# Optimization experiments

Measured on AMD Instinct MI355X. Metric: run time of the kernel, lower is better.

Reference implementation:

```python
import jax, jax.numpy as jnp
import numpy as np

B, N, L = 32, 50, 16384  # batch, n_templates, segment length
KT = 4096                # template kernel length


def conv1d(x, w, pad, groups=1):
    # x: [B, Cin, L], w: [Cout, Cin/groups, K] (torch layout)
    return jax.lax.conv_general_dilated(
        x, w, window_strides=(1,), padding=[(pad, pad)],
        dimension_numbers=('NCH', 'OIH', 'NCH'), feature_group_count=groups)


def maxpool3(x):
    # MaxPool1d(kernel=3, stride=3), floor mode (VALID)
    return jax.lax.reduce_window(x, -jnp.inf, jax.lax.max,
                                 (1, 1, 3), (1, 1, 3), 'VALID')


def pad_to(x, m):
    p = (-x.shape[-1]) % m
    pads = ((0, 0),) * (x.ndim - 1) + ((0, p),)
    return jnp.pad(x, pads)


def setup_inputs() -> dict:
    key = jax.random.key(0)
    ks = jax.random.split(key, 12)
    return dict(
        xi=jax.random.normal(ks[0], (B, 2, L), jnp.float32),
        S_t_m12=jax.random.normal(ks[1], (2, 1, L), jnp.float32) * 0.01,
        template=jax.random.normal(ks[2], (N, 2, KT), jnp.float32) * 0.01,
        hh_sqrt=jax.random.uniform(ks[3], (N, 2), jnp.float32) + 0.5,
        W1=jax.random.normal(ks[4], (16, 2, 3), jnp.float32) * 0.1,
        b1=jnp.zeros((16,), jnp.float32),
        W2=jax.random.normal(ks[5], (32, 16, 3), jnp.float32) * 0.1,
        b2=jnp.zeros((32,), jnp.float32),
        W3=jax.random.normal(ks[6], (32, 128), jnp.float32) * 0.1,
        b3=jnp.zeros((32,), jnp.float32),
        W4=jax.random.normal(ks[7], (2, 32), jnp.float32) * 0.1,
        b4=jnp.zeros((2,), jnp.float32),
    )


def reference(xi, S_t_m12, template, hh_sqrt, W1, b1, W2, b2, W3, b3, W4, b4):
    # Whitening matched filter: grouped conv with kernel length L
    y = conv1d(xi, S_t_m12, L - 1, groups=2)          # [B, 2, 2L-1]
    y = pad_to(y, L)                                   # [B, 2, 2L]
    # wrap-fold each channel: reshape(B,2,L).sum over the fold axis
    d_SA = y[:, 0].reshape(-1, 2, L).sum(1)[:, None, :]  # [B,1,L]
    d_SE = y[:, 1].reshape(-1, 2, L).sum(1)[:, None, :]
    h_SA = template[:, 0, :].reshape(-1, 1, KT)          # [N,1,KT]
    h_SE = template[:, 1, :].reshape(-1, 1, KT)
    dh_A = pad_to(conv1d(d_SA, h_SA, KT - 1), L).reshape(-1, N, 2, L).sum(2)  # [B,N,L]
    dh_E = pad_to(conv1d(d_SE, h_SE, KT - 1), L).reshape(-1, N, 2, L).sum(2)
    z = jnp.stack((dh_A, dh_E), -1).transpose(0, 2, 1, 3)  # [B,L,N,2]
    z = z / hh_sqrt                                         # broadcast [N,2]
    z = z.max(axis=1).transpose(0, 2, 1)                    # [B,2,N]
    # small CNN + MLP head
    h = maxpool3(jax.nn.sigmoid(conv1d(z, W1, 0) + b1[None, :, None]))  # [B,16,16]
    h = maxpool3(jax.nn.sigmoid(conv1d(h, W2, 0) + b2[None, :, None]))  # [B,32,4]
    h = h.reshape(h.shape[0], -1)                                        # [B,128]
    h = jax.nn.relu(h @ W3.T + b3)
    return h @ W4.T + b4                                                 # [B,2]
```

## Files before the change

### kernel.cpp

```cpp
#include <hip/hip_runtime.h>
#include <math.h>

#define L_LEN 16384
#define M_LEN 8192
#define KT_LEN 4096
#define BB 32
#define NTPL 50
#define SPEC_STRIDE 8224
#define NSIG 166
#define NT 512
#define PI_F 3.14159265358979323846f
#define C16 0.98078528040323044f
#define S16 0.19509032201612827f

typedef float cf2 __attribute__((ext_vector_type(2)));

__device__ __forceinline__ cf2 cmul(cf2 a, cf2 b) {
    cf2 byx = __builtin_shufflevector(b, b, 1, 0);
    return (cf2){a.x, a.x} * b + (cf2){-a.y, a.y} * byx;
}
__device__ __forceinline__ cf2 cmulc(cf2 a, cf2 b) {
    return a * (cf2){b.x, b.x} + (cf2){a.y, -a.x} * (cf2){b.y, b.y};
}
template<int SIGN>
__device__ __forceinline__ cf2 rot90(cf2 z) {
    return (SIGN < 0) ? (cf2){z.y, -z.x} : (cf2){-z.y, z.x};
}
template<int SIGN>
__device__ __forceinline__ cf2 ldT(const cf2* __restrict__ T, int idx) {
    cf2 t = T[idx];
    if (SIGN > 0) t.y = -t.y;
    return t;
}

__device__ __forceinline__ int swz(int i) { return i ^ (((i >> 5) & 15) << 1); }

__device__ __forceinline__ int pos(int f) {
    return ((f & 15) << 9) | (((f >> 4) & 15) << 5) |
           (((f >> 8) & 15) << 1) | ((f >> 12) & 1);
}

template<int SIGN>
__device__ __forceinline__ void dft16(cf2 x[16]) {
    const float S = (SIGN < 0) ? -1.f : 1.f;
    const cf2 w1 = {0.9238795325112867f, S * 0.3826834323650898f};
    const cf2 w2 = {0.7071067811865476f, S * 0.7071067811865476f};
    const cf2 w3 = {0.3826834323650898f, S * 0.9238795325112867f};
    cf2 v[16];
    #pragma unroll
    for (int n1 = 0; n1 < 4; ++n1) {
        cf2 a0 = x[n1], a1 = x[n1+4], a2 = x[n1+8], a3 = x[n1+12];
        cf2 t0 = a0 + a2, t2 = a0 - a2;
        cf2 t1 = a1 + a3, t3 = rot90<SIGN>(a1 - a3);
        cf2 u0 = t0 + t1, u1 = t2 + t3;
        cf2 u2 = t0 - t1, u3 = t2 - t3;
        if (n1 == 1) { u1 = cmul(u1, w1); u2 = cmul(u2, w2); u3 = cmul(u3, w3); }
        else if (n1 == 2) { u1 = cmul(u1, w2); u2 = rot90<SIGN>(u2);
                            u3 = rot90<SIGN>(cmul(u3, w2)); }
        else if (n1 == 3) { u1 = cmul(u1, w3); u2 = rot90<SIGN>(cmul(u2, w2));
                            u3 = -cmul(u3, w1); }
        v[0*4+n1] = u0; v[1*4+n1] = u1; v[2*4+n1] = u2; v[3*4+n1] = u3;
    }
    #pragma unroll
    for (int r = 0; r < 4; ++r) {
        cf2 a0 = v[r*4+0], a1 = v[r*4+1], a2 = v[r*4+2], a3 = v[r*4+3];
        cf2 t0 = a0 + a2, t2 = a0 - a2;
        cf2 t1 = a1 + a3, t3 = rot90<SIGN>(a1 - a3);
        x[r]    = t0 + t1; x[r+4]  = t2 + t3;
        x[r+8]  = t0 - t1; x[r+12] = t2 - t3;
    }
}

template<int SIGN>
__device__ __forceinline__ void butterfly16(cf2* A, const int idx[16], cf2 w1) {
    cf2 x[16];
    #pragma unroll
    for (int n = 0; n < 16; ++n) x[n] = A[idx[n]];
    dft16<SIGN>(x);
    A[idx[0]] = x[0];
    A[idx[1]] = cmul(x[1], w1);
    const cf2 w2 = cmul(w1, w1);
    A[idx[2]] = cmul(x[2], w2);
    const cf2 w3 = cmul(w1, w2);
    A[idx[3]] = cmul(x[3], w3);
    const cf2 w4 = cmul(w2, w2);
    A[idx[4]] = cmul(x[4], w4);
    A[idx[5]] = cmul(x[5], cmul(w1, w4));
    A[idx[6]] = cmul(x[6], cmul(w2, w4));
    A[idx[7]] = cmul(x[7], cmul(w3, w4));
    const cf2 w8 = cmul(w4, w4);
    A[idx[8]]  = cmul(x[8],  w8);
    A[idx[9]]  = cmul(x[9],  cmul(w1, w8));
    A[idx[10]] = cmul(x[10], cmul(w2, w8));
    A[idx[11]] = cmul(x[11], cmul(w3, w8));
    const cf2 w12 = cmul(w4, w8);
    A[idx[12]] = cmul(x[12], w12);
    A[idx[13]] = cmul(x[13], cmul(w1, w12));
    A[idx[14]] = cmul(x[14], cmul(w2, w12));
    A[idx[15]] = cmul(x[15], cmul(w3, w12));
}


__global__ __launch_bounds__(NT, 4)
void fwd_fft_kernel(const float* __restrict__ xi, const float* __restrict__ w,
                    const float* __restrict__ tmpl, cf2* __restrict__ Tw,
                    cf2* __restrict__ spec) {
    __shared__ __attribute__((aligned(16))) cf2 A[M_LEN];
    const int sig = blockIdx.x;
    const int tid = threadIdx.x;

    if (sig >= NSIG) {
        const int k = (sig - NSIG) * NT + tid;
        const double a = -M_PI * (double)k / 8192.0;
        Tw[k] = (cf2){(float)cos(a), (float)sin(a)};
        return;
    }

    const float* src;
    int nre;
    if (sig < 64)      { src = xi   + sig * L_LEN;         nre = L_LEN; }
    else if (sig < 66) { src = w    + (sig - 64) * L_LEN;  nre = L_LEN; }
    else               { src = tmpl + (sig - 66) * KT_LEN; nre = KT_LEN; }
    const int nc = nre >> 1;
    const float4* s4 = (const float4*)src;
    const int g0 = tid ^ ((tid >> 4) & 15);
    #pragma unroll
    for (int m = 0; m < 8; ++m) {
        const int u = 2*tid + 1024*m;
        float4 vv = (u < nc) ? s4[tid + 512*m] : make_float4(0.f, 0.f, 0.f, 0.f);
        ((float4*)A)[g0 + 512*m] = vv;
    }
    __syncthreads();

    {
        int idx[16]; const int b0 = swz(tid);
        #pragma unroll
        for (int n = 0; n < 16; ++n) idx[n] = b0 + 512*n;
        float sn, cs; __sincosf(-PI_F * (float)(2*tid) / 8192.f, &sn, &cs);
        butterfly16<-1>(A, idx, (cf2){cs, sn});
    }
    __syncthreads();
    {
        const int blk = tid >> 5, j = tid & 31, jb = blk*512;
        int idx[16];
        #pragma unroll
        for (int n = 0; n < 16; ++n) idx[n] = jb + 32*n + (j ^ (2*n));
        float sn, cs; __sincosf(-PI_F * (float)(32*j) / 8192.f, &sn, &cs);
        butterfly16<-1>(A, idx, (cf2){cs, sn});
    }
    __syncthreads();
    {
        const int blk = tid >> 1, j = tid & 1;
        const int xv = (blk & 15) << 1, b3 = blk*32 + j;
        int idx[16];
        #pragma unroll
        for (int n = 0; n < 16; ++n) idx[n] = b3 + ((2*n) ^ xv);
        cf2 w1 = j ? (cf2){C16, -S16} : (cf2){1.f, 0.f};
        butterfly16<-1>(A, idx, w1);
    }
    __syncthreads();
    #pragma unroll
    for (int m = 0; m < 8; ++m) {
        float4 pq = ((float4*)A)[g0 + 512*m];
        ((float4*)A)[g0 + 512*m] = make_float4(pq.x + pq.z, pq.y + pq.w,
                                               pq.x - pq.z, pq.y - pq.w);
    }
    __syncthreads();

    cf2* out = spec + (size_t)sig * SPEC_STRIDE;
    #pragma unroll
    for (int m = 0; m < 16; ++m) {
        const int f = tid + 512*m;
        const int fb = (M_LEN - f) & (M_LEN - 1);
        cf2 Za = A[swz(pos(f))];
        cf2 Zb = A[swz(pos(fb))];
        cf2 E = (cf2){0.5f*(Za.x + Zb.x), 0.5f*(Za.y - Zb.y)};
        cf2 D = (cf2){Za.x - Zb.x, Za.y + Zb.y};
        cf2 O = (cf2){0.5f*D.y, -0.5f*D.x};
        float sn, cs;
        __sincosf(-PI_F * (float)f / 8192.f, &sn, &cs);
        cf2 TO = (cf2){cs*O.x - sn*O.y, cs*O.y + sn*O.x};
        out[f] = E + TO;
    }
    if (tid == 0) {
        cf2 Za = A[swz(0)];
        out[M_LEN] = (cf2){Za.x - Za.y, 0.f};
    }
}

__global__ __launch_bounds__(512)
void premul_kernel(const cf2* __restrict__ T, cf2* __restrict__ spec) {
    const int bc = blockIdx.x;
    const int tid = threadIdx.x;
    const int c = bc & 1;
    cf2* Xs = spec + (size_t)bc * SPEC_STRIDE;
    const cf2* Ws = spec + (size_t)(64 + c) * SPEC_STRIDE;
    const int r = tid & 3;
    for (int f = tid; f <= M_LEN; f += 512) {
        cf2 t = cmulc(Xs[f], Ws[f]);
        cf2 p = T[(2*f) & (L_LEN - 1)];
        cf2 s = cmulc(t, p);
        cf2 o;
        if (r == 0)      o = s;
        else if (r == 1) o = (cf2){s.y, -s.x};
        else if (r == 2) o = -s;
        else             o = (cf2){-s.y, s.x};
        Xs[f] = o;
    }
}

__global__ __launch_bounds__(NT, 4)
void inv_fft_kernel(const cf2* __restrict__ spec, const cf2* __restrict__ T,
                    const float* __restrict__ hh, float* __restrict__ zarr) {
    __shared__ __attribute__((aligned(16))) cf2 A[M_LEN];
    const int idx0 = blockIdx.x;
    const int c = idx0 & 1;
    const int n = (idx0 >> 1) % NTPL;
    const int b = idx0 / (2 * NTPL);
    const int tid = threadIdx.x;

    const cf2* Ds = spec + (size_t)(b*2 + c)      * SPEC_STRIDE;
    const cf2* Hs = spec + (size_t)(66 + n*2 + c) * SPEC_STRIDE;
    const float4* D4 = (const float4*)Ds;
    const float4* H4 = (const float4*)Hs;
    const float4* T4 = (const float4*)T;
    const int g0 = tid ^ ((tid >> 4) & 15);

    #pragma unroll
    for (int m = 0; m < 4; ++m) {
        const int u = 2*tid + 1024*m;
        float4 df = D4[tid + 512*m], hf = H4[tid + 512*m];
        cf2 Sa0 = cmulc((cf2){df.x, df.y}, (cf2){hf.x, hf.y});
        cf2 Sa1 = cmulc((cf2){df.z, df.w}, (cf2){hf.z, hf.w});
        cf2 Sb0 = cmulc(Ds[M_LEN - u],     Hs[M_LEN - u]);
        cf2 Sb1 = cmulc(Ds[M_LEN - 1 - u], Hs[M_LEN - 1 - u]);
        float4 tw = T4[tid + 512*m];
        float cs0 = tw.x, sn0 = -tw.y;
        float Ex0 = 0.5f*(Sa0.x + Sb0.x), Ey0 = 0.5f*(Sa0.y - Sb0.y);
        float Dx0 = Sa0.x - Sb0.x,        Dy0 = Sa0.y + Sb0.y;
        float Ox0 = 0.5f*(cs0*Dx0 - sn0*Dy0), Oy0 = 0.5f*(cs0*Dy0 + sn0*Dx0);
        float cs1 = tw.z, sn1 = -tw.w;
        float Ex1 = 0.5f*(Sa1.x + Sb1.x), Ey1 = 0.5f*(Sa1.y - Sb1.y);
        float Dx1 = Sa1.x - Sb1.x,        Dy1 = Sa1.y + Sb1.y;
        float Ox1 = 0.5f*(cs1*Dx1 - sn1*Dy1), Oy1 = 0.5f*(cs1*Dy1 + sn1*Dx1);
        ((float4*)A)[g0 + 512*m] = make_float4(Ex0 - Oy0, Ey0 + Ox0,
                                               Ex1 - Oy1, Ey1 + Ox1);
        if (u > 0) A[swz(M_LEN - u)] = (cf2){Ex0 + Oy0, Ox0 - Ey0};
        A[swz(M_LEN - 1 - u)] = (cf2){Ex1 + Oy1, Ox1 - Ey1};
    }
    if (tid == 0) {
        cf2 S = cmulc(Ds[4096], Hs[4096]);
        A[swz(4096)] = (cf2){S.x, -S.y};
    }
    __syncthreads();

    {
        int idx[16]; const int b0 = swz(tid);
        #pragma unroll
        for (int nn = 0; nn < 16; ++nn) idx[nn] = b0 + 512*nn;
        butterfly16<+1>(A, idx, ldT<+1>(T, 2*tid));
    }
    __syncthreads();
    {
        const int blk = tid >> 5, j = tid & 31, jb = blk*512;
        int idx[16];
        #pragma unroll
        for (int nn = 0; nn < 16; ++nn) idx[nn] = jb + 32*nn + (j ^ (2*nn));
        butterfly16<+1>(A, idx, ldT<+1>(T, 32*j));
    }
    __syncthreads();

    float mx = -INFINITY;
    {
        const int blk = tid >> 1, j = tid & 1;
        const int xv = (blk & 15) << 1, b3 = blk*32 + j;
        cf2 x[16];
        #pragma unroll
        for (int nn = 0; nn < 16; ++nn) x[nn] = A[b3 + ((2*nn) ^ xv)];
        dft16<+1>(x);
        cf2 w1 = j ? (cf2){C16, S16} : (cf2){1.f, 0.f};
        auto acc = [&](cf2 z) {
            float qx = __shfl_xor(z.x, 1), qy = __shfl_xor(z.y, 1);
            float sx = z.x + qx, sy = z.y + qy;
            float dx = j ? qx - z.x : z.x - qx;
            float dy = j ? qy - z.y : z.y - qy;
            mx = fmaxf(mx, fmaxf(fmaxf(sx, sy), fmaxf(dx, dy)));
        };
        acc(x[0]);
        acc(cmul(x[1], w1));
        const cf2 w2 = cmul(w1, w1);
        acc(cmul(x[2], w2));
        const cf2 w3 = cmul(w1, w2);
        acc(cmul(x[3], w3));
        const cf2 w4 = cmul(w2, w2);
        acc(cmul(x[4], w4));
        acc(cmul(x[5], cmul(w1, w4)));
        acc(cmul(x[6], cmul(w2, w4)));
        acc(cmul(x[7], cmul(w3, w4)));
        const cf2 w8 = cmul(w4, w4);
        acc(cmul(x[8],  w8));
        acc(cmul(x[9],  cmul(w1, w8)));
        acc(cmul(x[10], cmul(w2, w8)));
        acc(cmul(x[11], cmul(w3, w8)));
        const cf2 w12 = cmul(w4, w8);
        acc(cmul(x[12], w12));
        acc(cmul(x[13], cmul(w1, w12)));
        acc(cmul(x[14], cmul(w2, w12)));
        acc(cmul(x[15], cmul(w3, w12)));
    }
    for (int off = 32; off > 0; off >>= 1)
        mx = fmaxf(mx, __shfl_xor(mx, off));
    __syncthreads();
    const int lane = tid & 63, wv = tid >> 6;
    float* redf = (float*)A;
    if (lane == 0) redf[wv] = mx;
    __syncthreads();
    if (tid == 0) {
        float mm = redf[0];
        for (int i = 1; i < NT/64; ++i) mm = fmaxf(mm, redf[i]);
        zarr[(b*2 + c)*NTPL + n] = mm / ((float)M_LEN * hh[n*2 + c]);
    }
}

__global__ __launch_bounds__(256)
void head_kernel(const float* __restrict__ zarr,
                 const float* __restrict__ W1, const float* __restrict__ b1,
                 const float* __restrict__ W2, const float* __restrict__ b2,
                 const float* __restrict__ W3, const float* __restrict__ b3,
                 const float* __restrict__ W4, const float* __restrict__ b4,
                 float* __restrict__ out) {
    __shared__ float zl[2][NTPL];
    __shared__ float s1[16][48];
    __shared__ float p1[16][16];
    __shared__ float s2[32][14];
    __shared__ float hflat[128];
    __shared__ float h1[32];
    const int b = blockIdx.x, tid = threadIdx.x;

    for (int i = tid; i < 2*NTPL; i += 256) zl[i/NTPL][i%NTPL] = zarr[b*2*NTPL + i];
    __syncthreads();
    for (int i = tid; i < 16*48; i += 256) {
        const int o = i / 48, t = i % 48;
        float acc = b1[o];
        #pragma unroll
        for (int cc = 0; cc < 2; ++cc)
            #pragma unroll
            for (int k = 0; k < 3; ++k)
                acc += zl[cc][t+k] * W1[o*6 + cc*3 + k];
        s1[o][t] = 1.f / (1.f + __expf(-acc));
    }
    __syncthreads();
    for (int i = tid; i < 16*16; i += 256) {
        const int o = i / 16, u = i % 16;
        p1[o][u] = fmaxf(fmaxf(s1[o][3*u], s1[o][3*u+1]), s1[o][3*u+2]);
    }
    __syncthreads();
    for (int i = tid; i < 32*14; i += 256) {
        const int o = i / 14, t = i % 14;
        float acc = b2[o];
        for (int cc = 0; cc < 16; ++cc)
            #pragma unroll
            for (int k = 0; k < 3; ++k)
                acc += p1[cc][t+k] * W2[o*48 + cc*3 + k];
        s2[o][t] = 1.f / (1.f + __expf(-acc));
    }
    __syncthreads();
    for (int i = tid; i < 128; i += 256) {
        const int o = i / 4, u = i % 4;
        hflat[i] = fmaxf(fmaxf(s2[o][3*u], s2[o][3*u+1]), s2[o][3*u+2]);
    }
    __syncthreads();
    if (tid < 32) {
        float acc = b3[tid];
        for (int j = 0; j < 128; ++j) acc += hflat[j] * W3[tid*128 + j];
        h1[tid] = fmaxf(acc, 0.f);
    }
    __syncthreads();
    if (tid < 2) {
        float acc = b4[tid];
        for (int j = 0; j < 32; ++j) acc += h1[j] * W4[tid*32 + j];
        out[b*2 + tid] = acc;
    }
}

extern "C" void kernel_launch(void* const* d_in, const int* in_sizes, int n_in,
                              void* d_out, int out_size, void* d_ws, size_t ws_size,
                              hipStream_t stream) {
    const float* xi   = (const float*)d_in[0];
    const float* Sw   = (const float*)d_in[1];
    const float* tmpl = (const float*)d_in[2];
    const float* hh   = (const float*)d_in[3];
    const float* W1   = (const float*)d_in[4];
    const float* b1   = (const float*)d_in[5];
    const float* W2   = (const float*)d_in[6];
    const float* b2   = (const float*)d_in[7];
    const float* W3   = (const float*)d_in[8];
    const float* b3   = (const float*)d_in[9];
    const float* W4   = (const float*)d_in[10];
    const float* b4   = (const float*)d_in[11];
    float* out = (float*)d_out;

    cf2* T16  = (cf2*)d_ws;
    cf2* spec = T16 + 16384;
    float* zarr = (float*)(spec + (size_t)NSIG * SPEC_STRIDE);

    fwd_fft_kernel<<<dim3(NSIG + 32), dim3(NT), 0, stream>>>(xi, Sw, tmpl, T16, spec);
    premul_kernel<<<dim3(64), dim3(512), 0, stream>>>(T16, spec);
    inv_fft_kernel<<<dim3(BB * NTPL * 2), dim3(NT), 0, stream>>>(spec, T16, hh, zarr);
    head_kernel<<<dim3(BB), dim3(256), 0, stream>>>(zarr, W1, b1, W2, b2, W3, b3, W4, b4, out);
}
```

Before: 165.1 us.

## Fold whitening premultiply into forward and inverse FFT kernels, drop premul launch

Removes the separate premul kernel. The phase-ramp and conjugation are folded into the whitening-filter spectrum at forward-FFT time, and the X*V product is computed on the fly inside every inverse-FFT block. The final radix stage in the inverse FFT is also swapped from a register dft16 with shuffle-based max to a shared-memory butterfly followed by a float4 scan for the max. This saves one launch and a read/write pass over the spectrum, at the cost of an extra spectrum load and complex multiply in each of the 3200 inverse blocks, plus an extra LDS round trip and barrier.

```diff
diff --git a/kernel.cpp b/kernel.cpp
--- a/kernel.cpp
+++ b/kernel.cpp
@@ -14,6 +14,7 @@
 #define S16 0.19509032201612827f
 
 typedef float cf2 __attribute__((ext_vector_type(2)));
+
 
 __device__ __forceinline__ cf2 cmul(cf2 a, cf2 b) {
     cf2 byx = __builtin_shufflevector(b, b, 1, 0);
@@ -121,6 +122,7 @@
     if (sig < 64)      { src = xi   + sig * L_LEN;         nre = L_LEN; }
     else if (sig < 66) { src = w    + (sig - 64) * L_LEN;  nre = L_LEN; }
     else               { src = tmpl + (sig - 66) * KT_LEN; nre = KT_LEN; }
+    const bool isW = (sig >= 64 && sig < 66);
     const int nc = nre >> 1;
     const float4* s4 = (const float4*)src;
     const int g0 = tid ^ ((tid >> 4) & 15);
@@ -179,33 +181,21 @@
         cf2 O = (cf2){0.5f*D.y, -0.5f*D.x};
         float sn, cs;
         __sincosf(-PI_F * (float)f / 8192.f, &sn, &cs);
-        cf2 TO = (cf2){cs*O.x - sn*O.y, cs*O.y + sn*O.x};
-        out[f] = E + TO;
+        cf2 val = E + (cf2){cs*O.x - sn*O.y, cs*O.y + sn*O.x};
+        if (isW) {
+            const int k = (4094 * f) & (L_LEN - 1);
+            float psn, pcs; __sincosf(-PI_F * (float)k / 8192.f, &psn, &pcs);
+            val = cmul((cf2){val.x, -val.y}, (cf2){pcs, psn});
+        }
+        out[f] = val;
     }
     if (tid == 0) {
         cf2 Za = A[swz(0)];
-        out[M_LEN] = (cf2){Za.x - Za.y, 0.f};
-    }
-}
-
-__global__ __launch_bounds__(512)
-void premul_kernel(const cf2* __restrict__ T, cf2* __restrict__ spec) {
-    const int bc = blockIdx.x;
-    const int tid = threadIdx.x;
-    const int c = bc & 1;
-    cf2* Xs = spec + (size_t)bc * SPEC_STRIDE;
-    const cf2* Ws = spec + (size_t)(64 + c) * SPEC_STRIDE;
-    const int r = tid & 3;
-    for (int f = tid; f <= M_LEN; f += 512) {
-        cf2 t = cmulc(Xs[f], Ws[f]);
-        cf2 p = T[(2*f) & (L_LEN - 1)];
-        cf2 s = cmulc(t, p);
-        cf2 o;
-        if (r == 0)      o = s;
-        else if (r == 1) o = (cf2){s.y, -s.x};
-        else if (r == 2) o = -s;
-        else             o = (cf2){-s.y, s.x};
-        Xs[f] = o;
+        cf2 val = (cf2){Za.x - Za.y, 0.f};
+        if (isW) {
+            val = (cf2){-val.x, 0.f};
+        }
+        out[M_LEN] = val;
     }
 }
 
@@ -219,9 +209,11 @@
     const int b = idx0 / (2 * NTPL);
     const int tid = threadIdx.x;
 
-    const cf2* Ds = spec + (size_t)(b*2 + c)      * SPEC_STRIDE;
+    const cf2* Xs = spec + (size_t)(b*2 + c)      * SPEC_STRIDE;
+    const cf2* Vs = spec + (size_t)(64 + c)       * SPEC_STRIDE;
     const cf2* Hs = spec + (size_t)(66 + n*2 + c) * SPEC_STRIDE;
-    const float4* D4 = (const float4*)Ds;
+    const float4* X4 = (const float4*)Xs;
+    const float4* V4 = (const float4*)Vs;
     const float4* H4 = (const float4*)Hs;
     const float4* T4 = (const float4*)T;
     const int g0 = tid ^ ((tid >> 4) & 15);
@@ -229,11 +221,11 @@
     #pragma unroll
     for (int m = 0; m < 4; ++m) {
         const int u = 2*tid + 1024*m;
-        float4 df = D4[tid + 512*m], hf = H4[tid + 512*m];
-        cf2 Sa0 = cmulc((cf2){df.x, df.y}, (cf2){hf.x, hf.y});
-        cf2 Sa1 = cmulc((cf2){df.z, df.w}, (cf2){hf.z, hf.w});
-        cf2 Sb0 = cmulc(Ds[M_LEN - u],     Hs[M_LEN - u]);
-        cf2 Sb1 = cmulc(Ds[M_LEN - 1 - u], Hs[M_LEN - 1 - u]);
+        float4 xf = X4[tid + 512*m], vf = V4[tid + 512*m], hf = H4[tid + 512*m];
+        cf2 Sa0 = cmulc(cmul((cf2){xf.x, xf.y}, (cf2){vf.x, vf.y}), (cf2){hf.x, hf.y});
+        cf2 Sa1 = cmulc(cmul((cf2){xf.z, xf.w}, (cf2){vf.z, vf.w}), (cf2){hf.z, hf.w});
+        cf2 Sb0 = cmulc(cmul(Xs[M_LEN - u],     Vs[M_LEN - u]),     Hs[M_LEN - u]);
+        cf2 Sb1 = cmulc(cmul(Xs[M_LEN - 1 - u], Vs[M_LEN - 1 - u]), Hs[M_LEN - 1 - u]);
         float4 tw = T4[tid + 512*m];
         float cs0 = tw.x, sn0 = -tw.y;
         float Ex0 = 0.5f*(Sa0.x + Sb0.x), Ey0 = 0.5f*(Sa0.y - Sb0.y);
@@ -249,7 +241,7 @@
         A[swz(M_LEN - 1 - u)] = (cf2){Ex1 + Oy1, Ox1 - Ey1};
     }
     if (tid == 0) {
-        cf2 S = cmulc(Ds[4096], Hs[4096]);
+        cf2 S = cmulc(cmul(Xs[4096], Vs[4096]), Hs[4096]);
         A[swz(4096)] = (cf2){S.x, -S.y};
     }
     __syncthreads();
@@ -269,48 +261,27 @@
         butterfly16<+1>(A, idx, ldT<+1>(T, 32*j));
     }
     __syncthreads();
-
-    float mx = -INFINITY;
     {
         const int blk = tid >> 1, j = tid & 1;
         const int xv = (blk & 15) << 1, b3 = blk*32 + j;
-        cf2 x[16];
-        #pragma unroll
-        for (int nn = 0; nn < 16; ++nn) x[nn] = A[b3 + ((2*nn) ^ xv)];
-        dft16<+1>(x);
+        int idx[16];
+        #pragma unroll
+        for (int nn = 0; nn < 16; ++nn) idx[nn] = b3 + ((2*nn) ^ xv);
         cf2 w1 = j ? (cf2){C16, S16} : (cf2){1.f, 0.f};
-        auto acc = [&](cf2 z) {
-            float qx = __shfl_xor(z.x, 1), qy = __shfl_xor(z.y, 1);
-            float sx = z.x + qx, sy = z.y + qy;
-            float dx = j ? qx - z.x : z.x - qx;
-            float dy = j ? qy - z.y : z.y - qy;
-            mx = fmaxf(mx, fmaxf(fmaxf(sx, sy), fmaxf(dx, dy)));
-        };
-        acc(x[0]);
-        acc(cmul(x[1], w1));
-        const cf2 w2 = cmul(w1, w1);
-        acc(cmul(x[2], w2));
-        const cf2 w3 = cmul(w1, w2);
-        acc(cmul(x[3], w3));
-        const cf2 w4 = cmul(w2, w2);
-        acc(cmul(x[4], w4));
-        acc(cmul(x[5], cmul(w1, w4)));
-        acc(cmul(x[6], cmul(w2, w4)));
-        acc(cmul(x[7], cmul(w3, w4)));
-        const cf2 w8 = cmul(w4, w4);
-        acc(cmul(x[8],  w8));
-        acc(cmul(x[9],  cmul(w1, w8)));
-        acc(cmul(x[10], cmul(w2, w8)));
-        acc(cmul(x[11], cmul(w3, w8)));
-        const cf2 w12 = cmul(w4, w8);
-        acc(cmul(x[12], w12));
-        acc(cmul(x[13], cmul(w1, w12)));
-        acc(cmul(x[14], cmul(w2, w12)));
-        acc(cmul(x[15], cmul(w3, w12)));
-    }
+        butterfly16<+1>(A, idx, w1);
+    }
+    __syncthreads();
+
+    float mx = -INFINITY;
+    #pragma unroll
+    for (int m = 0; m < 8; ++m) {
+        float4 pq = ((const float4*)A)[g0 + 512*m];
+        mx = fmaxf(mx, fmaxf(fmaxf(pq.x + pq.z, pq.y + pq.w),
+                             fmaxf(pq.x - pq.z, pq.y - pq.w)));
+    }
+    __syncthreads();
     for (int off = 32; off > 0; off >>= 1)
         mx = fmaxf(mx, __shfl_xor(mx, off));
-    __syncthreads();
     const int lane = tid & 63, wv = tid >> 6;
     float* redf = (float*)A;
     if (lane == 0) redf[wv] = mx;
@@ -405,7 +376,6 @@
     float* zarr = (float*)(spec + (size_t)NSIG * SPEC_STRIDE);
 
     fwd_fft_kernel<<<dim3(NSIG + 32), dim3(NT), 0, stream>>>(xi, Sw, tmpl, T16, spec);
-    premul_kernel<<<dim3(64), dim3(512), 0, stream>>>(T16, spec);
     inv_fft_kernel<<<dim3(BB * NTPL * 2), dim3(NT), 0, stream>>>(spec, T16, hh, zarr);
     head_kernel<<<dim3(BB), dim3(256), 0, stream>>>(zarr, W1, b1, W2, b2, W3, b3, W4, b4, out);
 }
```

Measured after the change: 157.7 us. 1.05x faster.
